# Performance work log

Hardware: AMD Instinct MI355X
Metric: run time of the kernel (lower is better)

The kernel has to match this reference:

```python
import jax, jax.numpy as jnp
import numpy as np

IN_CH = 256
NUM_ANCHORS = 9
NUM_CLASSES = 80
FEAT_SHAPES = [(4, IN_CH, 100, 100), (4, IN_CH, 50, 50), (4, IN_CH, 25, 25), (4, IN_CH, 13, 13), (4, IN_CH, 7, 7)]


def conv3x3(x, w, b):
    # x: [N,C,H,W], w: [O,I,3,3] (OIHW), stride 1, SAME padding
    y = jax.lax.conv_general_dilated(x, w, window_strides=(1, 1), padding='SAME',
                                     dimension_numbers=('NCHW', 'OIHW', 'NCHW'))
    return y + b[None, :, None, None]


def head_branch(x, conv_w, conv_b, out_w, out_b, K):
    for i in range(4):
        x = jax.nn.relu(conv3x3(x, conv_w[i], conv_b[i]))
    y = conv3x3(x, out_w, out_b)
    N, AK, H, W = y.shape
    A = AK // K
    return y.reshape(N, A, K, H, W).transpose(0, 3, 4, 1, 2).reshape(N, H * W * A, K)


def setup_inputs() -> dict:
    key = jax.random.key(0)
    ks = jax.random.split(key, 16)
    inp = {}
    for i, shp in enumerate(FEAT_SHAPES):
        inp[f'feat{i}'] = jax.random.normal(ks[i], shp, dtype=jnp.float32)
    std = 0.01  # torch init: normal(std=0.01), zero bias
    inp['cls_conv_w'] = jax.random.normal(ks[5], (4, IN_CH, IN_CH, 3, 3), dtype=jnp.float32) * std
    inp['cls_conv_b'] = jnp.zeros((4, IN_CH), dtype=jnp.float32)
    inp['cls_out_w'] = jax.random.normal(ks[6], (NUM_ANCHORS * NUM_CLASSES, IN_CH, 3, 3), dtype=jnp.float32) * std
    prior = 0.01
    inp['cls_out_b'] = jnp.full((NUM_ANCHORS * NUM_CLASSES,), -np.log((1.0 - prior) / prior), dtype=jnp.float32)
    inp['reg_conv_w'] = jax.random.normal(ks[7], (4, IN_CH, IN_CH, 3, 3), dtype=jnp.float32) * std
    inp['reg_conv_b'] = jnp.zeros((4, IN_CH), dtype=jnp.float32)
    inp['reg_out_w'] = jax.random.normal(ks[8], (NUM_ANCHORS * 4, IN_CH, 3, 3), dtype=jnp.float32) * std
    inp['reg_out_b'] = jnp.zeros((NUM_ANCHORS * 4,), dtype=jnp.float32)
    return inp


def reference(feat0, feat1, feat2, feat3, feat4,
              cls_conv_w, cls_conv_b, cls_out_w, cls_out_b,
              reg_conv_w, reg_conv_b, reg_out_w, reg_out_b):
    feats = [feat0, feat1, feat2, feat3, feat4]
    cls_logits = jnp.concatenate(
        [head_branch(f, cls_conv_w, cls_conv_b, cls_out_w, cls_out_b, NUM_CLASSES) for f in feats], axis=1)
    bbox_regression = jnp.concatenate(
        [head_branch(f, reg_conv_w, reg_conv_b, reg_out_w, reg_out_b, 4) for f in feats], axis=1)
    return cls_logits, bbox_regression
```

## Files before the change

### kernel.cpp

```cpp
#include <hip/hip_runtime.h>


typedef __bf16 v8bf __attribute__((ext_vector_type(8)));
typedef float f32x4 __attribute__((ext_vector_type(4)));

__device__ __forceinline__ v8bf zero8() {
  v8bf v;
#pragma unroll
  for (int j = 0; j < 8; ++j) v[j] = (__bf16)0.0f;
  return v;
}

__device__ __forceinline__ void glds16(const void* g, void* l) {
  __builtin_amdgcn_global_load_lds((const __attribute__((address_space(1))) unsigned int*)g,
                                   (__attribute__((address_space(3))) unsigned int*)l, 16, 0, 0);
}

struct Geo { int W, H, HW, pbase, obC, obR, t; };

__device__ __forceinline__ Geo decode128(int r) {
  Geo g;
  if (r < 79)       { g.W=100;g.H=100;g.HW=10000;g.pbase=0;     g.obC=0;       g.obR=0;      g.t=r; }
  else if (r < 99)  { g.W=50; g.H=50; g.HW=2500; g.pbase=40000; g.obC=7200000; g.obR=360000; g.t=r-79; }
  else if (r < 104) { g.W=25; g.H=25; g.HW=625;  g.pbase=50000; g.obC=9000000; g.obR=450000; g.t=r-99; }
  else if (r < 106) { g.W=13; g.H=13; g.HW=169;  g.pbase=52500; g.obC=9450000; g.obR=472500; g.t=r-104; }
  else              { g.W=7;  g.H=7;  g.HW=49;   g.pbase=53176; g.obC=9571680; g.obR=478584; g.t=r-106; }
  return g;
}
__device__ __forceinline__ Geo decode96(int r) {
  Geo g;
  if (r < 105)      { g.W=100;g.H=100;g.HW=10000;g.pbase=0;     g.obC=0;       g.obR=0;      g.t=r; }
  else if (r < 132) { g.W=50; g.H=50; g.HW=2500; g.pbase=40000; g.obC=7200000; g.obR=360000; g.t=r-105; }
  else if (r < 139) { g.W=25; g.H=25; g.HW=625;  g.pbase=50000; g.obC=9000000; g.obR=450000; g.t=r-132; }
  else if (r < 141) { g.W=13; g.H=13; g.HW=169;  g.pbase=52500; g.obC=9450000; g.obR=472500; g.t=r-139; }
  else              { g.W=7;  g.H=7;  g.HW=49;   g.pbase=53176; g.obC=9571680; g.obR=478584; g.t=r-141; }
  return g;
}

__global__ __launch_bounds__(256)
void prep_in(const float* __restrict__ f0, const float* __restrict__ f1,
             const float* __restrict__ f2, const float* __restrict__ f3,
             const float* __restrict__ f4, __bf16* __restrict__ dst)
{
  int g = blockIdx.x * 256 + threadIdx.x;
  if (g >= 1712000) return;
  int cg = g / 53500;
  int pix = g - cg * 53500;
  const float* s; int HW, hw, n;
  if (pix < 40000)      { s = f0; HW = 10000; int p = pix;         n = p / 10000; hw = p - n * 10000; }
  else if (pix < 50000) { s = f1; HW = 2500;  int p = pix - 40000; n = p / 2500;  hw = p - n * 2500;  }
  else if (pix < 52500) { s = f2; HW = 625;   int p = pix - 50000; n = p / 625;   hw = p - n * 625;   }
  else if (pix < 53176) { s = f3; HW = 169;   int p = pix - 52500; n = p / 169;   hw = p - n * 169;   }
  else                  { s = f4; HW = 49;    int p = pix - 53176; n = p / 49;    hw = p - n * 49;    }
  const float* sp = s + (n * 256 + cg * 8) * HW + hw;
  v8bf v;
#pragma unroll
  for (int j = 0; j < 8; ++j) v[j] = (__bf16)sp[j * HW];
  *(v8bf*)(dst + (size_t)pix * 256 + cg * 8) = v;
}

__global__ __launch_bounds__(256)
void prep_w_all(const float* __restrict__ cls_w, const float* __restrict__ reg_w,
                const float* __restrict__ cls_ow, const float* __restrict__ reg_ow,
                __bf16* __restrict__ wb)
{
  int t = blockIdx.x * 256 + threadIdx.x;
  const float* src; __bf16* dst; int CO, within;
  if (t < 589824) {
    int tensor = t / 73728; within = t % 73728;
    src = tensor < 4 ? cls_w + tensor * 589824 : reg_w + (tensor - 4) * 589824;
    dst = wb + (size_t)tensor * 589824; CO = 256;
  } else if (t < 811008) {
    within = t - 589824; src = cls_ow; dst = wb + 8 * 589824; CO = 720;
  } else {
    within = t - 811008; src = reg_ow; dst = wb + 8 * 589824 + 1769472; CO = 36;
  }
  int p = within & 3; int xx = within >> 2;
  int co = xx & 127; xx >>= 7;
  int tap = xx % 9; xx /= 9;
  int cc = xx & 7; int nt = xx >> 3;
  int l = p ^ ((co >> 1) & 3);
  int cog = nt * 128 + co;
  v8bf v = zero8();
  if (cog < CO) {
    const float* sp = src + ((size_t)cog * 256 + cc * 32 + l * 8) * 9 + tap;
#pragma unroll
    for (int j = 0; j < 8; ++j) v[j] = (__bf16)sp[j * 9];
  }
  *(v8bf*)(dst + ((size_t)(((nt * 8 + cc) * 9 + tap) * 128 + co) * 32 + p * 8)) = v;
}

__device__ __forceinline__ void conv_core_t(const char* __restrict__ wsbase,
    unsigned so, unsigned zpoff, const char* __restrict__ wnt,
    int W, int H, int p0, int npx, f32x4 (&acc)[3][4])
{
  __shared__ __align__(16) char ldsA[28672];
  __shared__ __align__(16) char ldsB[24576];
  const int Wp = W + 2;
  const int pend = p0 + npx - 1;
  const int rowlo = p0 / W - 1;
  const int tid = threadIdx.x, lane = tid & 63, wv = tid >> 6;
  const int wn = wv & 1, wm = wv >> 1, la = lane & 15, kg = lane >> 4;

  unsigned offA[7];
#pragma unroll
  for (int j = 0; j < 7; ++j) {
    int pos = (wv * 7 + j) * 16 + (lane >> 2);
    int h = pos / Wp;
    int wc = pos - h * Wp - 1;
    int ar = rowlo + h;
    int pl = (lane & 3) ^ ((pos >> 1) & 3);
    bool ok = (ar >= 0) & (ar < H) & (wc >= 0) & (wc < W);
    offA[j] = ok ? (so + (unsigned)(ar * W + wc) * 512u + (unsigned)pl * 16u)
                 : (zpoff + (unsigned)(lane & 3) * 16u);
  }

  int pos0[3], fvalid[3];
#pragma unroll
  for (int f = 0; f < 3; ++f) {
    int fg = wm * 3 + f;
    fvalid[f] = (fg * 16 < npx);
    int p = p0 + fg * 16 + la; if (p > pend) p = pend;
    int h = p / W;
    pos0[f] = (h - rowlo) * Wp + (p - h * W + 1);
  }

  int boff[4];
#pragma unroll
  for (int nj = 0; nj < 4; ++nj) {
    int co = wn * 64 + nj * 16 + la;
    boff[nj] = (co << 6) + ((kg << 4) ^ (((co >> 1) & 3) << 4));
  }

  const char* bq = wnt + wv * 2048 + lane * 16;
  char* bd = (char*)ldsB + wv * 2048;

#pragma unroll
  for (int j = 0; j < 7; ++j) { glds16(wsbase + offA[j], (char*)ldsA + (wv * 7 + j) * 1024); offA[j] += 64u; }
  glds16(bq, bd); glds16(bq + 1024, bd + 1024);
  glds16(bq + 8192, bd + 8192); glds16(bq + 9216, bd + 9216);

  for (int cc = 0; cc < 8; ++cc) {
#pragma unroll
    for (int tap = 0; tap < 9; ++tap) {
      if (tap == 8) {
        if (cc == 7) { asm volatile("s_waitcnt vmcnt(0)" ::: "memory"); }
        else         { asm volatile("s_waitcnt vmcnt(2)" ::: "memory"); }
      } else         { asm volatile("s_waitcnt vmcnt(2)" ::: "memory"); }
      __builtin_amdgcn_s_barrier();
      if (tap == 0 && cc > 0) {
#pragma unroll
        for (int j = 0; j < 7; ++j) { glds16(wsbase + offA[j], (char*)ldsA + (wv * 7 + j) * 1024); offA[j] += 64u; }
        const char* bs = bq + (cc * 9 + 2) * 8192;
        glds16(bs, bd + 16384); glds16(bs + 1024, bd + 17408);
        asm volatile("s_waitcnt vmcnt(2)" ::: "memory");
        __builtin_amdgcn_s_barrier();
      } else {
        int q = cc * 9 + tap;
        if (q < 70) {
          const char* bs = bq + (q + 2) * 8192;
          char* d = bd + ((tap + 2) % 3) * 8192;
          glds16(bs, d); glds16(bs + 1024, d + 1024);
        }
      }
      const char* bbuf = (const char*)ldsB + (tap % 3) * 8192;
      v8bf bfr[4];
#pragma unroll
      for (int nj = 0; nj < 4; ++nj) bfr[nj] = *(const v8bf*)(bbuf + boff[nj]);
      const int dh = tap / 3 - 1, dw = tap % 3 - 1;
      const int dt = dh * Wp + dw;
      v8bf afr[3];
#pragma unroll
      for (int f = 0; f < 3; ++f)
        if (fvalid[f]) {
          int pos = pos0[f] + dt;
          afr[f] = *(const v8bf*)((const char*)ldsA + ((pos << 6) + ((kg << 4) ^ (((pos >> 1) & 3) << 4))));
        }
      __builtin_amdgcn_s_setprio(1);
#pragma unroll
      for (int f = 0; f < 3; ++f)
        if (fvalid[f])
#pragma unroll
          for (int nj = 0; nj < 4; ++nj)
            acc[f][nj] = __builtin_amdgcn_mfma_f32_16x16x32_bf16(afr[f], bfr[nj], acc[f][nj], 0, 0, 0);
      __builtin_amdgcn_s_setprio(0);
    }
  }
}

__device__ __forceinline__ void conv_core_o(const char* __restrict__ wsbase,
    unsigned so, unsigned zpoff, const char* __restrict__ wnt,
    int W, int H, int p0, int npx, f32x4 (&acc)[4][4])
{
  __shared__ __align__(16) char ldsA[32768];
  __shared__ __align__(16) char ldsB[16384];
  const int Wp = W + 2;
  const int pend = p0 + npx - 1;
  const int rowlo = p0 / W - 1;
  const int tid = threadIdx.x, lane = tid & 63, wv = tid >> 6;
  const int wn = wv & 1, wm = wv >> 1, la = lane & 15, kg = lane >> 4;
  const int i0 = wv * 8;

  unsigned offA[8];
#pragma unroll
  for (int j = 0; j < 8; ++j) {
    int pos = (i0 + j) * 16 + (lane >> 2);
    int h = pos / Wp;
    int wc = pos - h * Wp - 1;
    int ar = rowlo + h;
    int pl = (lane & 3) ^ ((pos >> 1) & 3);
    bool ok = (ar >= 0) & (ar < H) & (wc >= 0) & (wc < W);
    offA[j] = ok ? (so + (unsigned)(ar * W + wc) * 512u + (unsigned)pl * 16u)
                 : (zpoff + (unsigned)(lane & 3) * 16u);
  }

  int pos0[4], fvalid[4];
#pragma unroll
  for (int f = 0; f < 4; ++f) {
    int fg = wm * 4 + f;
    fvalid[f] = (fg * 16 < npx);
    int p = p0 + fg * 16 + la; if (p > pend) p = pend;
    int h = p / W;
    pos0[f] = (h - rowlo) * Wp + (p - h * W + 1);
  }

  int boff[4];
#pragma unroll
  for (int nj = 0; nj < 4; ++nj) {
    int co = wn * 64 + nj * 16 + la;
    boff[nj] = (co << 6) + ((kg << 4) ^ (((co >> 1) & 3) << 4));
  }

  const char* bq = wnt + wv * 2048 + lane * 16;
  char* bd = (char*)ldsB + wv * 2048;

#define ISSUE_AO() do { _Pragma("unroll") \
    for (int j = 0; j < 8; ++j) { glds16(wsbase + offA[j], (char*)ldsA + (i0 + j) * 1024); offA[j] += 64u; } } while (0)
#define ISSUE_BO(q_, buf_) do { const char* s_ = bq + (q_) * 8192; \
    char* d_ = bd + (buf_) * 8192; \
    glds16(s_, d_); glds16(s_ + 1024, d_ + 1024); } while (0)

  ISSUE_AO();
  ISSUE_BO(0, 0);
  int pb = 0;

  for (int cc = 0; cc < 8; ++cc) {
#pragma unroll
    for (int tap = 0; tap < 9; ++tap) {
      __syncthreads();
      int q = cc * 9 + tap;
      if (q < 71) ISSUE_BO(q + 1, pb ^ 1);
      v8bf bfr[4];
#pragma unroll
      for (int nj = 0; nj < 4; ++nj) bfr[nj] = *(const v8bf*)((const char*)ldsB + pb * 8192 + boff[nj]);
      const int dh = tap / 3 - 1, dw = tap % 3 - 1;
      const int dt = dh * Wp + dw;
      v8bf afr[4];
#pragma unroll
      for (int f = 0; f < 4; ++f)
        if (fvalid[f]) {
          int pos = pos0[f] + dt;
          afr[f] = *(const v8bf*)((const char*)ldsA + ((pos << 6) + ((kg << 4) ^ (((pos >> 1) & 3) << 4))));
        }
#pragma unroll
      for (int f = 0; f < 4; ++f)
        if (fvalid[f])
#pragma unroll
          for (int nj = 0; nj < 4; ++nj)
            acc[f][nj] = __builtin_amdgcn_mfma_f32_16x16x32_bf16(afr[f], bfr[nj], acc[f][nj], 0, 0, 0);
      pb ^= 1;
      if (tap == 8 && cc < 7) { __syncthreads(); ISSUE_AO(); }
    }
  }
#undef ISSUE_AO
#undef ISSUE_BO
}

__global__ __launch_bounds__(256, 2)
void conv_tower(const char* __restrict__ wsbase,
                unsigned so0, __bf16* __restrict__ dst0, const __bf16* __restrict__ w0, const float* __restrict__ b0,
                unsigned so1, __bf16* __restrict__ dst1, const __bf16* __restrict__ w1, const float* __restrict__ b1,
                unsigned zpoff, int half)
{
  int bid = blockIdx.x;
  int br = bid >= half;
  bid -= br ? half : 0;
  unsigned soff = br ? so1 : so0;
  __bf16* dst = br ? dst1 : dst0;
  const __bf16* wt = br ? w1 : w0;
  const float* bias = br ? b1 : b0;

  int x = bid & 7, slot = bid >> 3;
  int nt = slot & 1, mtl = slot >> 1;
  int mt = x + (mtl << 3);
  int n = mt / 142, r = mt - n * 142;
  Geo g = decode96(r);
  int p0 = g.t * 96;
  int npx = g.HW - p0; if (npx > 96) npx = 96;
  unsigned so = soff + (unsigned)(g.pbase + n * g.HW) * 512u;

  f32x4 acc[3][4];
#pragma unroll
  for (int f = 0; f < 3; ++f)
#pragma unroll
    for (int j = 0; j < 4; ++j)
#pragma unroll
      for (int k = 0; k < 4; ++k) acc[f][j][k] = 0.0f;

  conv_core_t(wsbase, so, zpoff, (const char*)(wt + nt * 294912), g.W, g.H, p0, npx, acc);

  int lane = threadIdx.x & 63, wv = threadIdx.x >> 6;
  int wm = wv >> 1, wn = wv & 1, la = lane & 15, kg = lane >> 4;
  size_t pixbase = (size_t)(g.pbase + n * g.HW + p0);
#pragma unroll
  for (int f = 0; f < 3; ++f) {
    int fg = wm * 3 + f;
    if (fg * 16 < npx) {
#pragma unroll
      for (int nj = 0; nj < 4; ++nj) {
        int cob = nt * 128 + wn * 64 + nj * 16 + la;
        float bs = bias[cob];
#pragma unroll
        for (int rr = 0; rr < 4; ++rr) {
          int pl = fg * 16 + kg * 4 + rr;
          if (pl < npx)
            dst[((pixbase + pl) << 8) + cob] = (__bf16)fmaxf(acc[f][nj][rr] + bs, 0.0f);
        }
      }
    }
  }
}

__global__ __launch_bounds__(256, 3)
void conv_cls_out(const char* __restrict__ wsbase, unsigned soA,
                  float* __restrict__ out, const __bf16* __restrict__ wco,
                  const float* __restrict__ bco, unsigned zpoff)
{
  int bid0 = blockIdx.x;
  int bid = (bid0 & 7) * 321 + (bid0 >> 3);
  int nt = bid % 6, mt = bid / 6;
  int n = mt / 107, r = mt - n * 107;
  Geo g = decode128(r);
  int p0 = g.t << 7;
  int npx = g.HW - p0; if (npx > 128) npx = 128;
  unsigned so = soA + (unsigned)(g.pbase + n * g.HW) * 512u;

  f32x4 acc[4][4];
#pragma unroll
  for (int f = 0; f < 4; ++f)
#pragma unroll
    for (int j = 0; j < 4; ++j)
#pragma unroll
      for (int k = 0; k < 4; ++k) acc[f][j][k] = 0.0f;

  conv_core_o(wsbase, so, zpoff, (const char*)(wco + nt * 294912), g.W, g.H, p0, npx, acc);

  int lane = threadIdx.x & 63, wv = threadIdx.x >> 6;
  int wm = wv >> 1, wn = wv & 1, la = lane & 15, kg = lane >> 4;
#pragma unroll
  for (int f = 0; f < 4; ++f) {
    int fg = wm * 4 + f;
    if (fg * 16 < npx) {
#pragma unroll
      for (int nj = 0; nj < 4; ++nj) {
        int cob = nt * 128 + wn * 64 + nj * 16 + la;
        if (cob < 720) {
          float bs = bco[cob];
#pragma unroll
          for (int rr = 0; rr < 4; ++rr) {
            int pl = fg * 16 + kg * 4 + rr;
            if (pl < npx) {
              int pix = p0 + pl;
              out[(size_t)n * 9606960 + g.obC + (size_t)pix * 720 + cob] = acc[f][nj][rr] + bs;
            }
          }
        }
      }
    }
  }
}

__global__ __launch_bounds__(256, 3)
void conv_reg_out(const char* __restrict__ wsbase, unsigned soA,
                  float* __restrict__ out, const __bf16* __restrict__ wro,
                  const float* __restrict__ bro, unsigned zpoff)
{
  int mt = blockIdx.x;
  int n = mt / 107, r = mt - n * 107;
  Geo g = decode128(r);
  int p0 = g.t << 7;
  int npx = g.HW - p0; if (npx > 128) npx = 128;
  unsigned so = soA + (unsigned)(g.pbase + n * g.HW) * 512u;

  f32x4 acc[4][4];
#pragma unroll
  for (int f = 0; f < 4; ++f)
#pragma unroll
    for (int j = 0; j < 4; ++j)
#pragma unroll
      for (int k = 0; k < 4; ++k) acc[f][j][k] = 0.0f;

  conv_core_o(wsbase, so, zpoff, (const char*)wro, g.W, g.H, p0, npx, acc);

  int lane = threadIdx.x & 63, wv = threadIdx.x >> 6;
  int wm = wv >> 1, wn = wv & 1, la = lane & 15, kg = lane >> 4;
#pragma unroll
  for (int f = 0; f < 4; ++f) {
    int fg = wm * 4 + f;
    if (fg * 16 < npx) {
#pragma unroll
      for (int nj = 0; nj < 4; ++nj) {
        int cob = wn * 64 + nj * 16 + la;
        if (cob < 36) {
#pragma unroll
          for (int rr = 0; rr < 4; ++rr) {
            int pl = fg * 16 + kg * 4 + rr;
            if (pl < npx) {
              int pix = p0 + pl;
              out[38427840 + (size_t)n * 480348 + g.obR + (size_t)pix * 36 + cob] = acc[f][nj][rr] + bro[cob];
            }
          }
        }
      }
    }
  }
}

extern "C" void kernel_launch(void* const* d_in, const int* in_sizes, int n_in,
                              void* d_out, int out_size, void* d_ws, size_t ws_size,
                              hipStream_t stream) {
  (void)in_sizes; (void)n_in; (void)out_size;
  const float* feat0 = (const float*)d_in[0];
  const float* feat1 = (const float*)d_in[1];
  const float* feat2 = (const float*)d_in[2];
  const float* feat3 = (const float*)d_in[3];
  const float* feat4 = (const float*)d_in[4];
  const float* cls_w  = (const float*)d_in[5];
  const float* cls_b  = (const float*)d_in[6];
  const float* cls_ow = (const float*)d_in[7];
  const float* cls_ob = (const float*)d_in[8];
  const float* reg_w  = (const float*)d_in[9];
  const float* reg_b  = (const float*)d_in[10];
  const float* reg_ow = (const float*)d_in[11];
  const float* reg_ob = (const float*)d_in[12];
  float* out = (float*)d_out;

  const size_t ACT = 13663232;
  const size_t WSEG = 6782976;
  const char* wsbase = (const char*)d_ws;
  __bf16* base = (__bf16*)d_ws;

  bool fused = ws_size >= (5 * ACT + WSEG + 4096) * 2;
  int nact = fused ? 5 : 3;
  __bf16* A = base + ACT;
  __bf16* B = base + 2 * ACT;
  __bf16* C = fused ? base + 3 * ACT : A;
  __bf16* D = fused ? base + 4 * ACT : B;
  __bf16* wb = base + nact * ACT;

  __bf16* w_cls[4], *w_reg[4];
  for (int li = 0; li < 4; ++li) { w_cls[li] = wb + (size_t)li * 589824; w_reg[li] = wb + (size_t)(4 + li) * 589824; }
  __bf16* wco = wb + 8 * 589824;
  __bf16* wro = wco + 1769472;
  __bf16* zp = wro + 294912;

  unsigned off_in = 0;
  unsigned off_A = (unsigned)(ACT * 2);
  unsigned off_B = (unsigned)(ACT * 4);
  unsigned off_C = fused ? (unsigned)(ACT * 6) : off_A;
  unsigned off_D = fused ? (unsigned)(ACT * 8) : off_B;
  unsigned off_zp = (unsigned)((nact * ACT + WSEG) * 2);

  hipMemsetAsync(zp, 0, 8192, stream);
  prep_in<<<6688, 256, 0, stream>>>(feat0, feat1, feat2, feat3, feat4, base);
  prep_w_all<<<3312, 256, 0, stream>>>(cls_w, reg_w, cls_ow, reg_ow, wb);

  if (fused) {
    conv_tower<<<2272, 256, 0, stream>>>(wsbase, off_in, A, w_cls[0], cls_b + 0,   off_in, C, w_reg[0], reg_b + 0,   off_zp, 1136);
    conv_tower<<<2272, 256, 0, stream>>>(wsbase, off_A,  B, w_cls[1], cls_b + 256, off_C,  D, w_reg[1], reg_b + 256, off_zp, 1136);
    conv_tower<<<2272, 256, 0, stream>>>(wsbase, off_B,  A, w_cls[2], cls_b + 512, off_D,  C, w_reg[2], reg_b + 512, off_zp, 1136);
    conv_tower<<<2272, 256, 0, stream>>>(wsbase, off_C,  D, w_reg[3], reg_b + 768, off_A,  B, w_cls[3], cls_b + 768, off_zp, 1136);
    conv_cls_out<<<2568, 256, 0, stream>>>(wsbase, off_B, out, wco, cls_ob, off_zp);
    conv_reg_out<<<428, 256, 0, stream>>>(wsbase, off_D, out, wro, reg_ob, off_zp);
  } else {
    conv_tower<<<1136, 256, 0, stream>>>(wsbase, off_in, A, w_cls[0], cls_b + 0,   off_in, A, w_cls[0], cls_b, off_zp, 1136);
    conv_tower<<<1136, 256, 0, stream>>>(wsbase, off_A,  B, w_cls[1], cls_b + 256, off_A,  B, w_cls[1], cls_b, off_zp, 1136);
    conv_tower<<<1136, 256, 0, stream>>>(wsbase, off_B,  A, w_cls[2], cls_b + 512, off_B,  A, w_cls[2], cls_b, off_zp, 1136);
    conv_tower<<<1136, 256, 0, stream>>>(wsbase, off_A,  B, w_cls[3], cls_b + 768, off_A,  B, w_cls[3], cls_b, off_zp, 1136);
    conv_cls_out<<<2568, 256, 0, stream>>>(wsbase, off_B, out, wco, cls_ob, off_zp);
    conv_tower<<<1136, 256, 0, stream>>>(wsbase, off_in, A, w_reg[0], reg_b + 0,   off_in, A, w_reg[0], reg_b, off_zp, 1136);
    conv_tower<<<1136, 256, 0, stream>>>(wsbase, off_A,  B, w_reg[1], reg_b + 256, off_A,  B, w_reg[1], reg_b, off_zp, 1136);
    conv_tower<<<1136, 256, 0, stream>>>(wsbase, off_B,  A, w_reg[2], reg_b + 512, off_B,  A, w_reg[2], reg_b, off_zp, 1136);
    conv_tower<<<1136, 256, 0, stream>>>(wsbase, off_A,  B, w_reg[3], reg_b + 768, off_A,  B, w_reg[3], reg_b, off_zp, 1136);
    conv_reg_out<<<428, 256, 0, stream>>>(wsbase, off_B, out, wro, reg_ob, off_zp);
  }
}
```

Baseline: 995.2 us.

## Widen cls output conv tile to 256 channels with 512-thread blocks

The class-output convolution now uses 512-thread blocks that each compute a 128-pixel by 256-output-channel tile instead of 128x128. The weight prep for the class-output weights is rewritten to a 256-wide channel layout to match. The kernel is inlined with its own triple-buffered weight pipeline and a larger LDS footprint. Each block now loads its activation tile once for twice as many output channels, which is meant to cut repeated activation traffic. The cost is more LDS per block and a different occupancy trade-off.

```diff
diff --git a/kernel.cpp b/kernel.cpp
--- a/kernel.cpp
+++ b/kernel.cpp
@@ -65,29 +65,52 @@
                 __bf16* __restrict__ wb)
 {
   int t = blockIdx.x * 256 + threadIdx.x;
-  const float* src; __bf16* dst; int CO, within;
   if (t < 589824) {
-    int tensor = t / 73728; within = t % 73728;
-    src = tensor < 4 ? cls_w + tensor * 589824 : reg_w + (tensor - 4) * 589824;
-    dst = wb + (size_t)tensor * 589824; CO = 256;
+    int tensor = t / 73728, within = t % 73728;
+    const float* src = tensor < 4 ? cls_w + tensor * 589824 : reg_w + (tensor - 4) * 589824;
+    __bf16* dst = wb + (size_t)tensor * 589824;
+    int p = within & 3; int xx = within >> 2;
+    int co = xx & 127; xx >>= 7;
+    int tap = xx % 9; xx /= 9;
+    int cc = xx & 7; int nt = xx >> 3;
+    int l = p ^ ((co >> 1) & 3);
+    int cog = nt * 128 + co;
+    v8bf v = zero8();
+    const float* sp = src + ((size_t)cog * 256 + cc * 32 + l * 8) * 9 + tap;
+#pragma unroll
+    for (int j = 0; j < 8; ++j) v[j] = (__bf16)sp[j * 9];
+    *(v8bf*)(dst + ((size_t)(((nt * 8 + cc) * 9 + tap) * 128 + co) * 32 + p * 8)) = v;
   } else if (t < 811008) {
-    within = t - 589824; src = cls_ow; dst = wb + 8 * 589824; CO = 720;
+    int within = t - 589824;
+    int p = within & 3; int xx = within >> 2;
+    int co = xx & 255; xx >>= 8;
+    int tap = xx % 9; xx /= 9;
+    int cc = xx & 7; int nt = xx >> 3;
+    int l = p ^ ((co >> 1) & 3);
+    int cog = nt * 256 + co;
+    v8bf v = zero8();
+    if (cog < 720) {
+      const float* sp = cls_ow + ((size_t)cog * 256 + cc * 32 + l * 8) * 9 + tap;
+#pragma unroll
+      for (int j = 0; j < 8; ++j) v[j] = (__bf16)sp[j * 9];
+    }
+    *(v8bf*)(wb + (size_t)8 * 589824 + (size_t)nt * 589824 +
+             ((size_t)((cc * 9 + tap) * 256 + co) * 32 + p * 8)) = v;
   } else {
-    within = t - 811008; src = reg_ow; dst = wb + 8 * 589824 + 1769472; CO = 36;
-  }
-  int p = within & 3; int xx = within >> 2;
-  int co = xx & 127; xx >>= 7;
-  int tap = xx % 9; xx /= 9;
-  int cc = xx & 7; int nt = xx >> 3;
-  int l = p ^ ((co >> 1) & 3);
-  int cog = nt * 128 + co;
-  v8bf v = zero8();
-  if (cog < CO) {
-    const float* sp = src + ((size_t)cog * 256 + cc * 32 + l * 8) * 9 + tap;
-#pragma unroll
-    for (int j = 0; j < 8; ++j) v[j] = (__bf16)sp[j * 9];
-  }
-  *(v8bf*)(dst + ((size_t)(((nt * 8 + cc) * 9 + tap) * 128 + co) * 32 + p * 8)) = v;
+    int within = t - 811008;
+    int p = within & 3; int xx = within >> 2;
+    int co = xx & 127; xx >>= 7;
+    int tap = xx % 9; int cc = xx / 9;
+    int l = p ^ ((co >> 1) & 3);
+    v8bf v = zero8();
+    if (co < 36) {
+      const float* sp = reg_ow + ((size_t)co * 256 + cc * 32 + l * 8) * 9 + tap;
+#pragma unroll
+      for (int j = 0; j < 8; ++j) v[j] = (__bf16)sp[j * 9];
+    }
+    *(v8bf*)(wb + (size_t)8 * 589824 + 1769472 +
+             ((size_t)((cc * 9 + tap) * 128 + co) * 32 + p * 8)) = v;
+  }
 }
 
 __device__ __forceinline__ void conv_core_t(const char* __restrict__ wsbase,
@@ -331,19 +354,63 @@
   }
 }
 
-__global__ __launch_bounds__(256, 3)
+__global__ __launch_bounds__(512, 4)
 void conv_cls_out(const char* __restrict__ wsbase, unsigned soA,
                   float* __restrict__ out, const __bf16* __restrict__ wco,
                   const float* __restrict__ bco, unsigned zpoff)
 {
+  __shared__ __align__(16) char ldsA[32768];
+  __shared__ __align__(16) char ldsB[49152];
+
   int bid0 = blockIdx.x;
-  int bid = (bid0 & 7) * 321 + (bid0 >> 3);
-  int nt = bid % 6, mt = bid / 6;
+  int x = bid0 & 7, i = bid0 >> 3;
+  int w = (x < 4) ? (x * 161 + i) : (644 + (x - 4) * 160 + i);
+  int nt = w % 3, mt = w / 3;
   int n = mt / 107, r = mt - n * 107;
   Geo g = decode128(r);
   int p0 = g.t << 7;
   int npx = g.HW - p0; if (npx > 128) npx = 128;
   unsigned so = soA + (unsigned)(g.pbase + n * g.HW) * 512u;
+  const char* wnt = (const char*)(wco + (size_t)nt * 589824);
+
+  const int Wp = g.W + 2;
+  const int pend = p0 + npx - 1;
+  const int rowlo = p0 / g.W - 1;
+  const int tid = threadIdx.x, lane = tid & 63, wv = tid >> 6;
+  const int wm = wv >> 2, wn = wv & 3, la = lane & 15, kg = lane >> 4;
+
+  unsigned offA[4];
+#pragma unroll
+  for (int j = 0; j < 4; ++j) {
+    int pos = (wv * 4 + j) * 16 + (lane >> 2);
+    int h = pos / Wp;
+    int wc = pos - h * Wp - 1;
+    int ar = rowlo + h;
+    int pl = (lane & 3) ^ ((pos >> 1) & 3);
+    bool ok = (ar >= 0) & (ar < g.H) & (wc >= 0) & (wc < g.W);
+    offA[j] = ok ? (so + (unsigned)(ar * g.W + wc) * 512u + (unsigned)pl * 16u)
+                 : (zpoff + (unsigned)(lane & 3) * 16u);
+  }
+
+  int pos0[4], fvalid[4];
+#pragma unroll
+  for (int f = 0; f < 4; ++f) {
+    int fg = wm * 4 + f;
+    fvalid[f] = (fg * 16 < npx);
+    int p = p0 + fg * 16 + la; if (p > pend) p = pend;
+    int h = p / g.W;
+    pos0[f] = (h - rowlo) * Wp + (p - h * g.W + 1);
+  }
+
+  int boff[4];
+#pragma unroll
+  for (int nj = 0; nj < 4; ++nj) {
+    int co = wn * 64 + nj * 16 + la;
+    boff[nj] = (co << 6) + ((kg << 4) ^ (((co >> 1) & 3) << 4));
+  }
+
+  const char* bq = wnt + wv * 2048 + lane * 16;
+  char* bd = (char*)ldsB + wv * 2048;
 
   f32x4 acc[4][4];
 #pragma unroll
@@ -353,17 +420,65 @@
 #pragma unroll
       for (int k = 0; k < 4; ++k) acc[f][j][k] = 0.0f;
 
-  conv_core_o(wsbase, so, zpoff, (const char*)(wco + nt * 294912), g.W, g.H, p0, npx, acc);
-
-  int lane = threadIdx.x & 63, wv = threadIdx.x >> 6;
-  int wm = wv >> 1, wn = wv & 1, la = lane & 15, kg = lane >> 4;
+#pragma unroll
+  for (int j = 0; j < 4; ++j) { glds16(wsbase + offA[j], (char*)ldsA + (wv * 4 + j) * 1024); offA[j] += 64u; }
+  glds16(bq, bd); glds16(bq + 1024, bd + 1024);
+  glds16(bq + 16384, bd + 16384); glds16(bq + 17408, bd + 17408);
+
+  for (int cc = 0; cc < 8; ++cc) {
+#pragma unroll
+    for (int tap = 0; tap < 9; ++tap) {
+      if (tap == 8) {
+        if (cc == 7) { asm volatile("s_waitcnt vmcnt(0)" ::: "memory"); }
+        else         { asm volatile("s_waitcnt vmcnt(2)" ::: "memory"); }
+      } else         { asm volatile("s_waitcnt vmcnt(2)" ::: "memory"); }
+      __builtin_amdgcn_s_barrier();
+      if (tap == 0 && cc > 0) {
+#pragma unroll
+        for (int j = 0; j < 4; ++j) { glds16(wsbase + offA[j], (char*)ldsA + (wv * 4 + j) * 1024); offA[j] += 64u; }
+        const char* bs = bq + (size_t)(cc * 9 + 2) * 16384;
+        glds16(bs, bd + 32768); glds16(bs + 1024, bd + 33792);
+        asm volatile("s_waitcnt vmcnt(2)" ::: "memory");
+        __builtin_amdgcn_s_barrier();
+      } else {
+        int q = cc * 9 + tap;
+        if (q < 70) {
+          const char* bs = bq + (size_t)(q + 2) * 16384;
+          char* d = bd + ((tap + 2) % 3) * 16384;
+          glds16(bs, d); glds16(bs + 1024, d + 1024);
+        }
+      }
+      const char* bbuf = (const char*)ldsB + (tap % 3) * 16384;
+      v8bf bfr[4];
+#pragma unroll
+      for (int nj = 0; nj < 4; ++nj) bfr[nj] = *(const v8bf*)(bbuf + boff[nj]);
+      const int dh = tap / 3 - 1, dw = tap % 3 - 1;
+      const int dt = dh * Wp + dw;
+      v8bf afr[4];
+#pragma unroll
+      for (int f = 0; f < 4; ++f)
+        if (fvalid[f]) {
+          int pos = pos0[f] + dt;
+          afr[f] = *(const v8bf*)((const char*)ldsA + ((pos << 6) + ((kg << 4) ^ (((pos >> 1) & 3) << 4))));
+        }
+      __builtin_amdgcn_s_setprio(1);
+#pragma unroll
+      for (int f = 0; f < 4; ++f)
+        if (fvalid[f])
+#pragma unroll
+          for (int nj = 0; nj < 4; ++nj)
+            acc[f][nj] = __builtin_amdgcn_mfma_f32_16x16x32_bf16(afr[f], bfr[nj], acc[f][nj], 0, 0, 0);
+      __builtin_amdgcn_s_setprio(0);
+    }
+  }
+
 #pragma unroll
   for (int f = 0; f < 4; ++f) {
     int fg = wm * 4 + f;
     if (fg * 16 < npx) {
 #pragma unroll
       for (int nj = 0; nj < 4; ++nj) {
-        int cob = nt * 128 + wn * 64 + nj * 16 + la;
+        int cob = nt * 256 + wn * 64 + nj * 16 + la;
         if (cob < 720) {
           float bs = bco[cob];
 #pragma unroll
@@ -480,14 +595,14 @@
     conv_tower<<<2272, 256, 0, stream>>>(wsbase, off_A,  B, w_cls[1], cls_b + 256, off_C,  D, w_reg[1], reg_b + 256, off_zp, 1136);
     conv_tower<<<2272, 256, 0, stream>>>(wsbase, off_B,  A, w_cls[2], cls_b + 512, off_D,  C, w_reg[2], reg_b + 512, off_zp, 1136);
     conv_tower<<<2272, 256, 0, stream>>>(wsbase, off_C,  D, w_reg[3], reg_b + 768, off_A,  B, w_cls[3], cls_b + 768, off_zp, 1136);
-    conv_cls_out<<<2568, 256, 0, stream>>>(wsbase, off_B, out, wco, cls_ob, off_zp);
+    conv_cls_out<<<1284, 512, 0, stream>>>(wsbase, off_B, out, wco, cls_ob, off_zp);
     conv_reg_out<<<428, 256, 0, stream>>>(wsbase, off_D, out, wro, reg_ob, off_zp);
   } else {
     conv_tower<<<1136, 256, 0, stream>>>(wsbase, off_in, A, w_cls[0], cls_b + 0,   off_in, A, w_cls[0], cls_b, off_zp, 1136);
     conv_tower<<<1136, 256, 0, stream>>>(wsbase, off_A,  B, w_cls[1], cls_b + 256, off_A,  B, w_cls[1], cls_b, off_zp, 1136);
     conv_tower<<<1136, 256, 0, stream>>>(wsbase, off_B,  A, w_cls[2], cls_b + 512, off_B,  A, w_cls[2], cls_b, off_zp, 1136);
     conv_tower<<<1136, 256, 0, stream>>>(wsbase, off_A,  B, w_cls[3], cls_b + 768, off_A,  B, w_cls[3], cls_b, off_zp, 1136);
-    conv_cls_out<<<2568, 256, 0, stream>>>(wsbase, off_B, out, wco, cls_ob, off_zp);
+    conv_cls_out<<<1284, 512, 0, stream>>>(wsbase, off_B, out, wco, cls_ob, off_zp);
     conv_tower<<<1136, 256, 0, stream>>>(wsbase, off_in, A, w_reg[0], reg_b + 0,   off_in, A, w_reg[0], reg_b, off_zp, 1136);
     conv_tower<<<1136, 256, 0, stream>>>(wsbase, off_A,  B, w_reg[1], reg_b + 256, off_A,  B, w_reg[1], reg_b, off_zp, 1136);
     conv_tower<<<1136, 256, 0, stream>>>(wsbase, off_B,  A, w_reg[2], reg_b + 512, off_B,  A, w_reg[2], reg_b, off_zp, 1136);
```

Result: slower. 1.110 ms (+11.6%).
